# Kernel tuning notes

Hardware: AMD Instinct MI355X
Metric: run time of the kernel (lower is better)

## Reference

```python
import jax, jax.numpy as jnp
import numpy as np

S = 4096          # sequence length (must equal d_model due to the module's v-transpose bug)
D = 4096          # d_model; n_head = heads = 1, bs = 1
SCALE = 64.0      # scale_factor = sqrt(d_model)
W_STD = 0.02      # weight init scale to keep softmax logits sane


def setup_inputs() -> dict:
    k0 = jax.random.key(0)
    ks = jax.random.split(k0, 8)
    return {
        "query": jax.random.normal(ks[0], (1, S, D), jnp.float32),
        "key":   jax.random.normal(ks[1], (1, S, D), jnp.float32),
        "value": jax.random.normal(ks[2], (1, S, D), jnp.float32),
        "Wq": jax.random.normal(ks[3], (D, D), jnp.float32) * W_STD,
        "bq": jnp.zeros((D,), jnp.float32),
        "Wk": jax.random.normal(ks[4], (D, D), jnp.float32) * W_STD,
        "bk": jnp.zeros((D,), jnp.float32),
        "Wv": jax.random.normal(ks[5], (D, D), jnp.float32) * W_STD,
        "bv": jnp.zeros((D,), jnp.float32),
        "Wo": jax.random.normal(ks[6], (D, D), jnp.float32) * W_STD,
        "bo": jnp.zeros((D,), jnp.float32),
    }


def reference(query, key, value, Wq, bq, Wk, bk, Wv, bv, Wo, bo):
    # Linear projections (torch Linear: x @ W.T + b). n_head = 1, so out dim = D.
    q = query @ Wq.T + bq                       # [1, S, D]
    k = key   @ Wk.T + bk                       # [1, S, D]
    v = value @ Wv.T + bv                       # [1, S, D]
    # k.reshape(bs, heads, -1, d_model).transpose(2, 3) -> [1, 1, D, S]
    k4 = k.reshape(1, 1, S, D).transpose(0, 1, 3, 2)
    # v gets the SAME (buggy) transpose -> [1, 1, D, S]
    v4 = v.reshape(1, 1, S, D).transpose(0, 1, 3, 2)
    # q [1,S,D] broadcasts against k4 [1,1,D,S] -> scores [1,1,S,S]
    scores = jnp.matmul(q[:, None], k4) / SCALE
    attn = jax.nn.softmax(scores, axis=-1)      # [1, 1, S, S]
    # dropout_p = 0 / eval mode -> identity
    ctx = jnp.matmul(attn, v4)                  # [1, 1, S, D] (S == D)
    out = ctx @ Wo.T + bo + value[:, None]      # residual add, broadcast to [1,1,S,D]
    return out.reshape(1, -1, D)                # [1, S, D]
```

## Files before the change

### kernel.cpp

```cpp
#include <hip/hip_runtime.h>


typedef __attribute__((ext_vector_type(4))) float f32x4;
typedef __attribute__((ext_vector_type(8))) short short8;
typedef __attribute__((ext_vector_type(4))) unsigned short us4;

#define DIM 4096
#define NT  64

__device__ __forceinline__ unsigned short f2bf(float f) {
    unsigned int u = __builtin_bit_cast(unsigned int, f);
    u += 0x7fffu + ((u >> 16) & 1u);
    return (unsigned short)(u >> 16);
}

__device__ __forceinline__ void gll16(const void* g, void* l) {
    __builtin_amdgcn_global_load_lds(
        (const __attribute__((address_space(1))) unsigned int*)g,
        (__attribute__((address_space(3))) unsigned int*)l,
        16, 0, 0);
}

__global__ void cast_kernel(const float* __restrict__ in, unsigned short* __restrict__ out) {
    const size_t i = ((size_t)blockIdx.x * 256 + threadIdx.x) * 4;
    float4 x = *(const float4*)(in + i);
    us4 y;
    y.x = f2bf(x.x); y.y = f2bf(x.y); y.z = f2bf(x.z); y.w = f2bf(x.w);
    *(us4*)(out + i) = y;
}

template <int EPI>
__global__ __launch_bounds__(512, 2)
void gemm256(const unsigned short* __restrict__ A, const unsigned short* __restrict__ B,
             void* __restrict__ Cout, const float* __restrict__ bias,
             const float* __restrict__ res) {
    __shared__ alignas(16) char lds[131072];

    const int tid = threadIdx.x;
    const int w = tid >> 6, l = tid & 63;
    const int wr = w >> 2, wc = w & 3;

    const int bid = blockIdx.x;
    const int swz = (bid & 7) * 32 + (bid >> 3);
    const int row0 = (swz >> 4) << 8;
    const int col0 = (swz & 15) << 8;

    const int laneA  = (l & 15) * 64 + (((l >> 4) << 4) ^ ((l & 8) << 2));
    const int sl_row = l >> 2;
    const int sl_col = ((l & 3) << 3) ^ ((l & 32) ? 16 : 0);

    f32x4 acc[8][4];
    const f32x4 zero = {0.f, 0.f, 0.f, 0.f};
#pragma unroll
    for (int m = 0; m < 8; ++m)
#pragma unroll
        for (int n = 0; n < 4; ++n) acc[m][n] = zero;

    char* const ldsp = (char*)lds;

    auto stage = [&](const unsigned short* __restrict__ M, char* ldsMat, int rowbase,
                     int t, int h) {
        {
            const int rg = h * 8 + (w >> 1), cg = w & 1;
            gll16(M + (size_t)(rowbase + rg * 16 + sl_row) * DIM + t * 64 + cg * 32 + sl_col,
                  ldsMat + ((rg * 2 + cg) << 10));
        }
        {
            const int s = 8 + w;
            const int rg = h * 8 + (s >> 1), cg = s & 1;
            gll16(M + (size_t)(rowbase + rg * 16 + sl_row) * DIM + t * 64 + cg * 32 + sl_col,
                  ldsMat + ((rg * 2 + cg) << 10));
        }
    };

    stage(A, ldsp,          row0, 0, 0);
    stage(A, ldsp,          row0, 0, 1);
    stage(B, ldsp + 32768,  col0, 0, 0);
    stage(B, ldsp + 32768,  col0, 0, 1);
    stage(A, ldsp + 65536,  row0, 1, 0);
    asm volatile("s_waitcnt vmcnt(2)\ns_barrier" ::: "memory");

#pragma unroll 1
    for (int t = 0; t < NT; ++t) {
        const char* Ab = ldsp + (t & 1) * 65536;
        const char* Bb = Ab + 32768;
        const int t1 = (t + 1 < NT) ? t + 1 : NT - 1;
        const int t2 = (t + 2 < NT) ? t + 2 : NT - 1;
        char* A1 = ldsp + (t1 & 1) * 65536;
        char* B1 = A1 + 32768;
        char* A2 = ldsp + (t2 & 1) * 65536;

        const int aoff = wr * 16384 + laneA;
        const int boff = wc * 8192 + laneA;

        short8 alo[4][2], ahi[4][2], b0[2][2], b1[2][2];

#pragma unroll
        for (int n2 = 0; n2 < 2; ++n2)
#pragma unroll
            for (int ks = 0; ks < 2; ++ks)
                b0[n2][ks] = *(const short8*)(Bb + boff + ((n2 * 2 + ks) << 10));
#pragma unroll
        for (int m2 = 0; m2 < 4; ++m2)
#pragma unroll
            for (int ks = 0; ks < 2; ++ks)
                alo[m2][ks] = *(const short8*)(Ab + aoff + ((m2 * 2 + ks) << 10));
        stage(A, A1, row0, t1, 1);
        __builtin_amdgcn_s_setprio(1);
#pragma unroll
        for (int m2 = 0; m2 < 4; ++m2)
#pragma unroll
            for (int n2 = 0; n2 < 2; ++n2)
#pragma unroll
                for (int ks = 0; ks < 2; ++ks)
                    acc[m2][n2] = __builtin_amdgcn_mfma_f32_16x16x32_bf16(
                        alo[m2][ks], b0[n2][ks], acc[m2][n2], 0, 0, 0);
        __builtin_amdgcn_s_setprio(0);

#pragma unroll
        for (int n2 = 0; n2 < 2; ++n2)
#pragma unroll
            for (int ks = 0; ks < 2; ++ks)
                b1[n2][ks] = *(const short8*)(Bb + boff + (((2 + n2) * 2 + ks) << 10));
#pragma unroll
        for (int m2 = 0; m2 < 4; ++m2)
#pragma unroll
            for (int ks = 0; ks < 2; ++ks)
                ahi[m2][ks] = *(const short8*)(Ab + aoff + (((4 + m2) * 2 + ks) << 10));
        stage(B, B1, col0, t1, 0);
        __builtin_amdgcn_s_setprio(1);
#pragma unroll
        for (int m2 = 0; m2 < 4; ++m2)
#pragma unroll
            for (int n2 = 0; n2 < 2; ++n2)
#pragma unroll
                for (int ks = 0; ks < 2; ++ks)
                    acc[m2][2 + n2] = __builtin_amdgcn_mfma_f32_16x16x32_bf16(
                        alo[m2][ks], b1[n2][ks], acc[m2][2 + n2], 0, 0, 0);
        __builtin_amdgcn_s_setprio(0);

        asm volatile("s_barrier" ::: "memory");

        stage(B, B1, col0, t1, 1);
        __builtin_amdgcn_s_setprio(1);
#pragma unroll
        for (int m2 = 0; m2 < 4; ++m2)
#pragma unroll
            for (int n2 = 0; n2 < 2; ++n2)
#pragma unroll
                for (int ks = 0; ks < 2; ++ks)
                    acc[4 + m2][2 + n2] = __builtin_amdgcn_mfma_f32_16x16x32_bf16(
                        ahi[m2][ks], b1[n2][ks], acc[4 + m2][2 + n2], 0, 0, 0);
        __builtin_amdgcn_s_setprio(0);

        stage(A, A2, row0, t2, 0);
        __builtin_amdgcn_s_setprio(1);
#pragma unroll
        for (int m2 = 0; m2 < 4; ++m2)
#pragma unroll
            for (int n2 = 0; n2 < 2; ++n2)
#pragma unroll
                for (int ks = 0; ks < 2; ++ks)
                    acc[4 + m2][n2] = __builtin_amdgcn_mfma_f32_16x16x32_bf16(
                        ahi[m2][ks], b0[n2][ks], acc[4 + m2][n2], 0, 0, 0);
        __builtin_amdgcn_s_setprio(0);
        asm volatile("s_waitcnt vmcnt(2)\ns_barrier" ::: "memory");
    }
    asm volatile("s_waitcnt vmcnt(0)" ::: "memory");

#pragma unroll
    for (int mf = 0; mf < 8; ++mf) {
        const int grow0 = row0 + wr * 128 + mf * 16 + ((l >> 4) << 2);
#pragma unroll
        for (int nf = 0; nf < 4; ++nf) {
            const int gcol = col0 + wc * 64 + nf * 16 + (l & 15);
            float bias_v = 0.f;
            if constexpr (EPI != 1) {
                if (bias) bias_v = bias[gcol];
            }
#pragma unroll
            for (int r = 0; r < 4; ++r) {
                const size_t idx = (size_t)(grow0 + r) * DIM + gcol;
                const float x = acc[mf][nf][r] + bias_v;
                if constexpr (EPI == 0) {
                    ((unsigned short*)Cout)[idx] = f2bf(x);
                } else if constexpr (EPI == 1) {
                    ((float*)Cout)[idx] = x * 0.015625f;
                } else {
                    ((float*)Cout)[idx] = x + res[idx];
                }
            }
        }
    }
}

__global__ __launch_bounds__(256)
void softmax_kernel(const float* __restrict__ S, unsigned short* __restrict__ P) {
    const int row = blockIdx.x;
    const int t = threadIdx.x;
    const float* src = S + (size_t)row * DIM;

    float v[16];
#pragma unroll
    for (int i = 0; i < 16; ++i) v[i] = src[t + (i << 8)];

    float m = v[0];
#pragma unroll
    for (int i = 1; i < 16; ++i) m = fmaxf(m, v[i]);
#pragma unroll
    for (int off = 32; off > 0; off >>= 1) m = fmaxf(m, __shfl_xor(m, off));

    __shared__ float redm[4], reds[4];
    if ((t & 63) == 0) redm[t >> 6] = m;
    __syncthreads();
    m = fmaxf(fmaxf(redm[0], redm[1]), fmaxf(redm[2], redm[3]));

    float s = 0.f;
#pragma unroll
    for (int i = 0; i < 16; ++i) {
        v[i] = expf(v[i] - m);
        s += v[i];
    }
#pragma unroll
    for (int off = 32; off > 0; off >>= 1) s += __shfl_xor(s, off);
    if ((t & 63) == 0) reds[t >> 6] = s;
    __syncthreads();
    s = (reds[0] + reds[1]) + (reds[2] + reds[3]);

    const float inv = 1.0f / s;
    unsigned short* dst = P + (size_t)row * DIM;
#pragma unroll
    for (int i = 0; i < 16; ++i) dst[t + (i << 8)] = f2bf(v[i] * inv);
}

extern "C" void kernel_launch(void* const* d_in, const int* in_sizes, int n_in,
                              void* d_out, int out_size, void* d_ws, size_t ws_size,
                              hipStream_t stream) {
    const float* query = (const float*)d_in[0];
    const float* key   = (const float*)d_in[1];
    const float* value = (const float*)d_in[2];
    const float* Wq    = (const float*)d_in[3];
    const float* bq    = (const float*)d_in[4];
    const float* Wk    = (const float*)d_in[5];
    const float* bk    = (const float*)d_in[6];
    const float* Wv    = (const float*)d_in[7];
    const float* bv    = (const float*)d_in[8];
    const float* Wo    = (const float*)d_in[9];
    const float* bo    = (const float*)d_in[10];

    const size_t SZ = (size_t)DIM * DIM;
    unsigned short* qb   = (unsigned short*)d_ws;
    unsigned short* kb   = qb + SZ;
    unsigned short* vb   = kb + SZ;
    unsigned short* xb   = vb + SZ;
    unsigned short* wb   = xb + SZ;
    unsigned short* Pb   = wb + SZ;
    unsigned short* ctxb = Pb + SZ;
    float* scores = (float*)(ctxb + SZ);

    const dim3 cg(16384), cb(256);
    const dim3 gg(256), gb(512);

    cast_kernel<<<cg, cb, 0, stream>>>(query, xb);
    cast_kernel<<<cg, cb, 0, stream>>>(Wq, wb);
    gemm256<0><<<gg, gb, 0, stream>>>(xb, wb, qb, bq, nullptr);
    cast_kernel<<<cg, cb, 0, stream>>>(key, xb);
    cast_kernel<<<cg, cb, 0, stream>>>(Wk, wb);
    gemm256<0><<<gg, gb, 0, stream>>>(xb, wb, kb, bk, nullptr);
    cast_kernel<<<cg, cb, 0, stream>>>(value, xb);
    cast_kernel<<<cg, cb, 0, stream>>>(Wv, wb);
    gemm256<0><<<gg, gb, 0, stream>>>(xb, wb, vb, bv, nullptr);
    gemm256<1><<<gg, gb, 0, stream>>>(qb, kb, scores, nullptr, nullptr);
    softmax_kernel<<<4096, 256, 0, stream>>>(scores, Pb);
    gemm256<0><<<gg, gb, 0, stream>>>(Pb, vb, ctxb, nullptr, nullptr);
    cast_kernel<<<cg, cb, 0, stream>>>(Wo, wb);
    gemm256<2><<<gg, gb, 0, stream>>>(ctxb, wb, d_out, bo, value);
}
```

Baseline: 796.1 us.

## Switch GEMM to 32x32x16 bf16 MFMA with matching LDS layout

Replaces the 16x16x32 MFMA tiling with 32x32x16 bf16 MFMA instructions, so each wave holds 4x2 f32x16 accumulators instead of 8x4 f32x4. The global-to-LDS staging layout, the swizzled LDS read offsets and the epilogue row/column mapping are all rewritten to match the 32x32 operand format. The larger MFMA shape is meant to cut the instruction count and the LDS read traffic per FLOP. It also changes the bank-conflict behaviour and register usage.

```diff
diff --git a/kernel.cpp b/kernel.cpp
--- a/kernel.cpp
+++ b/kernel.cpp
@@ -1,7 +1,7 @@
 #include <hip/hip_runtime.h>
 
 
-typedef __attribute__((ext_vector_type(4))) float f32x4;
+typedef __attribute__((ext_vector_type(16))) float f32x16;
 typedef __attribute__((ext_vector_type(8))) short short8;
 typedef __attribute__((ext_vector_type(4))) unsigned short us4;
 
@@ -45,31 +45,30 @@
     const int row0 = (swz >> 4) << 8;
     const int col0 = (swz & 15) << 8;
 
-    const int laneA  = (l & 15) * 64 + (((l >> 4) << 4) ^ ((l & 8) << 2));
-    const int sl_row = l >> 2;
-    const int sl_col = ((l & 3) << 3) ^ ((l & 32) ? 16 : 0);
-
-    f32x4 acc[8][4];
-    const f32x4 zero = {0.f, 0.f, 0.f, 0.f};
-#pragma unroll
-    for (int m = 0; m < 8; ++m)
-#pragma unroll
-        for (int n = 0; n < 4; ++n) acc[m][n] = zero;
+    const int laneR = (l & 31) * 32 + (((l >> 5) ^ (l & 1)) << 4);
+    const int sg_row = l >> 1;
+    const int sg_k   = ((l & 1) ^ ((l >> 1) & 1)) << 3;
+
+    f32x16 acc[4][2];
+#pragma unroll
+    for (int m = 0; m < 4; ++m)
+#pragma unroll
+        for (int n = 0; n < 2; ++n)
+#pragma unroll
+            for (int r = 0; r < 16; ++r) acc[m][n][r] = 0.f;
 
     char* const ldsp = (char*)lds;
 
     auto stage = [&](const unsigned short* __restrict__ M, char* ldsMat, int rowbase,
                      int t, int h) {
-        {
-            const int rg = h * 8 + (w >> 1), cg = w & 1;
-            gll16(M + (size_t)(rowbase + rg * 16 + sl_row) * DIM + t * 64 + cg * 32 + sl_col,
-                  ldsMat + ((rg * 2 + cg) << 10));
-        }
-        {
-            const int s = 8 + w;
-            const int rg = h * 8 + (s >> 1), cg = s & 1;
-            gll16(M + (size_t)(rowbase + rg * 16 + sl_row) * DIM + t * 64 + cg * 32 + sl_col,
-                  ldsMat + ((rg * 2 + cg) << 10));
+        const int R = h * 4 + (w & 3);
+        const int grow = rowbase + R * 32 + sg_row;
+        const int Kg0 = (w >> 2) * 2;
+#pragma unroll
+        for (int j = 0; j < 2; ++j) {
+            const int Kg = Kg0 + j;
+            gll16(M + (size_t)grow * DIM + t * 64 + Kg * 16 + sg_k,
+                  ldsMat + ((R * 4 + Kg) << 10));
         }
     };
 
@@ -90,53 +89,45 @@
         char* B1 = A1 + 32768;
         char* A2 = ldsp + (t2 & 1) * 65536;
 
-        const int aoff = wr * 16384 + laneA;
-        const int boff = wc * 8192 + laneA;
-
-        short8 alo[4][2], ahi[4][2], b0[2][2], b1[2][2];
-
-#pragma unroll
-        for (int n2 = 0; n2 < 2; ++n2)
-#pragma unroll
-            for (int ks = 0; ks < 2; ++ks)
-                b0[n2][ks] = *(const short8*)(Bb + boff + ((n2 * 2 + ks) << 10));
-#pragma unroll
-        for (int m2 = 0; m2 < 4; ++m2)
-#pragma unroll
-            for (int ks = 0; ks < 2; ++ks)
-                alo[m2][ks] = *(const short8*)(Ab + aoff + ((m2 * 2 + ks) << 10));
+        const int aoff = wr * 16384 + laneR;
+        const int boff = wc * 8192 + laneR;
+
+        short8 alo[2][4], ahi[2][4], b0[4], b1[4];
+
+#pragma unroll
+        for (int ks = 0; ks < 4; ++ks)
+            b0[ks] = *(const short8*)(Bb + boff + (ks << 10));
+#pragma unroll
+        for (int mf = 0; mf < 2; ++mf)
+#pragma unroll
+            for (int ks = 0; ks < 4; ++ks)
+                alo[mf][ks] = *(const short8*)(Ab + aoff + (mf << 12) + (ks << 10));
         stage(A, A1, row0, t1, 1);
         __builtin_amdgcn_s_setprio(1);
 #pragma unroll
-        for (int m2 = 0; m2 < 4; ++m2)
-#pragma unroll
-            for (int n2 = 0; n2 < 2; ++n2)
-#pragma unroll
-                for (int ks = 0; ks < 2; ++ks)
-                    acc[m2][n2] = __builtin_amdgcn_mfma_f32_16x16x32_bf16(
-                        alo[m2][ks], b0[n2][ks], acc[m2][n2], 0, 0, 0);
-        __builtin_amdgcn_s_setprio(0);
-
-#pragma unroll
-        for (int n2 = 0; n2 < 2; ++n2)
-#pragma unroll
-            for (int ks = 0; ks < 2; ++ks)
-                b1[n2][ks] = *(const short8*)(Bb + boff + (((2 + n2) * 2 + ks) << 10));
-#pragma unroll
-        for (int m2 = 0; m2 < 4; ++m2)
-#pragma unroll
-            for (int ks = 0; ks < 2; ++ks)
-                ahi[m2][ks] = *(const short8*)(Ab + aoff + (((4 + m2) * 2 + ks) << 10));
+        for (int mf = 0; mf < 2; ++mf)
+#pragma unroll
+            for (int ks = 0; ks < 4; ++ks)
+                acc[mf][0] = __builtin_amdgcn_mfma_f32_32x32x16_bf16(
+                    alo[mf][ks], b0[ks], acc[mf][0], 0, 0, 0);
+        __builtin_amdgcn_s_setprio(0);
+
+#pragma unroll
+        for (int ks = 0; ks < 4; ++ks)
+            b1[ks] = *(const short8*)(Bb + boff + 4096 + (ks << 10));
+#pragma unroll
+        for (int mf = 0; mf < 2; ++mf)
+#pragma unroll
+            for (int ks = 0; ks < 4; ++ks)
+                ahi[mf][ks] = *(const short8*)(Ab + aoff + ((2 + mf) << 12) + (ks << 10));
         stage(B, B1, col0, t1, 0);
         __builtin_amdgcn_s_setprio(1);
 #pragma unroll
-        for (int m2 = 0; m2 < 4; ++m2)
-#pragma unroll
-            for (int n2 = 0; n2 < 2; ++n2)
-#pragma unroll
-                for (int ks = 0; ks < 2; ++ks)
-                    acc[m2][2 + n2] = __builtin_amdgcn_mfma_f32_16x16x32_bf16(
-                        alo[m2][ks], b1[n2][ks], acc[m2][2 + n2], 0, 0, 0);
+        for (int mf = 0; mf < 2; ++mf)
+#pragma unroll
+            for (int ks = 0; ks < 4; ++ks)
+                acc[mf][1] = __builtin_amdgcn_mfma_f32_32x32x16_bf16(
+                    alo[mf][ks], b1[ks], acc[mf][1], 0, 0, 0);
         __builtin_amdgcn_s_setprio(0);
 
         asm volatile("s_barrier" ::: "memory");
@@ -144,44 +135,41 @@
         stage(B, B1, col0, t1, 1);
         __builtin_amdgcn_s_setprio(1);
 #pragma unroll
-        for (int m2 = 0; m2 < 4; ++m2)
-#pragma unroll
-            for (int n2 = 0; n2 < 2; ++n2)
-#pragma unroll
-                for (int ks = 0; ks < 2; ++ks)
-                    acc[4 + m2][2 + n2] = __builtin_amdgcn_mfma_f32_16x16x32_bf16(
-                        ahi[m2][ks], b1[n2][ks], acc[4 + m2][2 + n2], 0, 0, 0);
+        for (int mf = 0; mf < 2; ++mf)
+#pragma unroll
+            for (int ks = 0; ks < 4; ++ks)
+                acc[2 + mf][1] = __builtin_amdgcn_mfma_f32_32x32x16_bf16(
+                    ahi[mf][ks], b1[ks], acc[2 + mf][1], 0, 0, 0);
         __builtin_amdgcn_s_setprio(0);
 
         stage(A, A2, row0, t2, 0);
         __builtin_amdgcn_s_setprio(1);
 #pragma unroll
-        for (int m2 = 0; m2 < 4; ++m2)
-#pragma unroll
-            for (int n2 = 0; n2 < 2; ++n2)
-#pragma unroll
-                for (int ks = 0; ks < 2; ++ks)
-                    acc[4 + m2][n2] = __builtin_amdgcn_mfma_f32_16x16x32_bf16(
-                        ahi[m2][ks], b0[n2][ks], acc[4 + m2][n2], 0, 0, 0);
+        for (int mf = 0; mf < 2; ++mf)
+#pragma unroll
+            for (int ks = 0; ks < 4; ++ks)
+                acc[2 + mf][0] = __builtin_amdgcn_mfma_f32_32x32x16_bf16(
+                    ahi[mf][ks], b0[ks], acc[2 + mf][0], 0, 0, 0);
         __builtin_amdgcn_s_setprio(0);
         asm volatile("s_waitcnt vmcnt(2)\ns_barrier" ::: "memory");
     }
     asm volatile("s_waitcnt vmcnt(0)" ::: "memory");
 
 #pragma unroll
-    for (int mf = 0; mf < 8; ++mf) {
-        const int grow0 = row0 + wr * 128 + mf * 16 + ((l >> 4) << 2);
-#pragma unroll
-        for (int nf = 0; nf < 4; ++nf) {
-            const int gcol = col0 + wc * 64 + nf * 16 + (l & 15);
+    for (int mf = 0; mf < 4; ++mf) {
+        const int grow_b = row0 + wr * 128 + mf * 32 + ((l >> 5) << 2);
+#pragma unroll
+        for (int nf = 0; nf < 2; ++nf) {
+            const int gcol = col0 + wc * 64 + nf * 32 + (l & 31);
             float bias_v = 0.f;
             if constexpr (EPI != 1) {
                 if (bias) bias_v = bias[gcol];
             }
 #pragma unroll
-            for (int r = 0; r < 4; ++r) {
-                const size_t idx = (size_t)(grow0 + r) * DIM + gcol;
-                const float x = acc[mf][nf][r] + bias_v;
+            for (int rg = 0; rg < 16; ++rg) {
+                const int grow = grow_b + (rg & 3) + ((rg >> 2) << 3);
+                const size_t idx = (size_t)grow * DIM + gcol;
+                const float x = acc[mf][nf][rg] + bias_v;
                 if constexpr (EPI == 0) {
                     ((unsigned short*)Cout)[idx] = f2bf(x);
                 } else if constexpr (EPI == 1) {
```

Result: slower. 913.4 us (+14.7%).

## Restructure GEMM main loop to prefetch next tile fragments and double-buffer B registers

Applied to the files above, without the earlier changes.

Reorganizes the bf16 MFMA GEMM main loop into a two-iteration unrolled body. The prologue stages two full K-tiles, and each step loads the next tile's alo/b0 fragments into registers before the final MFMA group. Global-to-LDS staging now targets tile t+2 in the just-consumed buffer, with adjusted waitcnt and barrier placement. The goal is to hide LDS read latency and cut barrier stalls, at the cost of more live registers (an extra b0 set) and a more delicate synchronisation scheme.

```diff
diff --git a/kernel.cpp b/kernel.cpp
--- a/kernel.cpp
+++ b/kernel.cpp
@@ -57,6 +57,13 @@
         for (int n = 0; n < 4; ++n) acc[m][n] = zero;
 
     char* const ldsp = (char*)lds;
+    char* const A0 = ldsp;
+    char* const B0 = ldsp + 32768;
+    char* const A1 = ldsp + 65536;
+    char* const B1 = ldsp + 98304;
+
+    const int aoff = wr * 16384 + laneA;
+    const int boff = wc * 8192 + laneA;
 
     auto stage = [&](const unsigned short* __restrict__ M, char* ldsMat, int rowbase,
                      int t, int h) {
@@ -73,39 +80,38 @@
         }
     };
 
-    stage(A, ldsp,          row0, 0, 0);
-    stage(A, ldsp,          row0, 0, 1);
-    stage(B, ldsp + 32768,  col0, 0, 0);
-    stage(B, ldsp + 32768,  col0, 0, 1);
-    stage(A, ldsp + 65536,  row0, 1, 0);
-    asm volatile("s_waitcnt vmcnt(2)\ns_barrier" ::: "memory");
-
-#pragma unroll 1
-    for (int t = 0; t < NT; ++t) {
-        const char* Ab = ldsp + (t & 1) * 65536;
-        const char* Bb = Ab + 32768;
-        const int t1 = (t + 1 < NT) ? t + 1 : NT - 1;
+    short8 alo[4][2], ahi[4][2], b1[2][2], b0A[2][2], b0B[2][2];
+
+    stage(A, A0, row0, 0, 0); stage(A, A0, row0, 0, 1);
+    stage(B, B0, col0, 0, 0); stage(B, B0, col0, 0, 1);
+    stage(A, A1, row0, 1, 0); stage(A, A1, row0, 1, 1);
+    stage(B, B1, col0, 1, 0); stage(B, B1, col0, 1, 1);
+    asm volatile("s_waitcnt vmcnt(8)\ns_barrier" ::: "memory");
+#pragma unroll
+    for (int m2 = 0; m2 < 4; ++m2)
+#pragma unroll
+        for (int ks = 0; ks < 2; ++ks)
+            alo[m2][ks] = *(const short8*)(A0 + aoff + ((m2 * 2 + ks) << 10));
+#pragma unroll
+    for (int n2 = 0; n2 < 2; ++n2)
+#pragma unroll
+        for (int ks = 0; ks < 2; ++ks)
+            b0A[n2][ks] = *(const short8*)(B0 + boff + ((n2 * 2 + ks) << 10));
+
+    auto body = [&](int t, char* Abuf, char* Bbuf, const char* An, const char* Bn,
+                    short8 (&b0c)[2][2], short8 (&b0n)[2][2]) {
         const int t2 = (t + 2 < NT) ? t + 2 : NT - 1;
-        char* A1 = ldsp + (t1 & 1) * 65536;
-        char* B1 = A1 + 32768;
-        char* A2 = ldsp + (t2 & 1) * 65536;
-
-        const int aoff = wr * 16384 + laneA;
-        const int boff = wc * 8192 + laneA;
-
-        short8 alo[4][2], ahi[4][2], b0[2][2], b1[2][2];
 
 #pragma unroll
         for (int n2 = 0; n2 < 2; ++n2)
 #pragma unroll
             for (int ks = 0; ks < 2; ++ks)
-                b0[n2][ks] = *(const short8*)(Bb + boff + ((n2 * 2 + ks) << 10));
-#pragma unroll
-        for (int m2 = 0; m2 < 4; ++m2)
-#pragma unroll
-            for (int ks = 0; ks < 2; ++ks)
-                alo[m2][ks] = *(const short8*)(Ab + aoff + ((m2 * 2 + ks) << 10));
-        stage(A, A1, row0, t1, 1);
+                b1[n2][ks] = *(const short8*)(Bbuf + boff + (((2 + n2) * 2 + ks) << 10));
+#pragma unroll
+        for (int m2 = 0; m2 < 4; ++m2)
+#pragma unroll
+            for (int ks = 0; ks < 2; ++ks)
+                ahi[m2][ks] = *(const short8*)(Abuf + aoff + (((4 + m2) * 2 + ks) << 10));
         __builtin_amdgcn_s_setprio(1);
 #pragma unroll
         for (int m2 = 0; m2 < 4; ++m2)
@@ -114,20 +120,12 @@
 #pragma unroll
                 for (int ks = 0; ks < 2; ++ks)
                     acc[m2][n2] = __builtin_amdgcn_mfma_f32_16x16x32_bf16(
-                        alo[m2][ks], b0[n2][ks], acc[m2][n2], 0, 0, 0);
-        __builtin_amdgcn_s_setprio(0);
-
-#pragma unroll
-        for (int n2 = 0; n2 < 2; ++n2)
-#pragma unroll
-            for (int ks = 0; ks < 2; ++ks)
-                b1[n2][ks] = *(const short8*)(Bb + boff + (((2 + n2) * 2 + ks) << 10));
-#pragma unroll
-        for (int m2 = 0; m2 < 4; ++m2)
-#pragma unroll
-            for (int ks = 0; ks < 2; ++ks)
-                ahi[m2][ks] = *(const short8*)(Ab + aoff + (((4 + m2) * 2 + ks) << 10));
-        stage(B, B1, col0, t1, 0);
+                        alo[m2][ks], b0c[n2][ks], acc[m2][n2], 0, 0, 0);
+        __builtin_amdgcn_s_setprio(0);
+        asm volatile("s_barrier" ::: "memory");
+
+        stage(A, Abuf, row0, t2, 0);
+        stage(A, Abuf, row0, t2, 1);
         __builtin_amdgcn_s_setprio(1);
 #pragma unroll
         for (int m2 = 0; m2 < 4; ++m2)
@@ -139,9 +137,7 @@
                         alo[m2][ks], b1[n2][ks], acc[m2][2 + n2], 0, 0, 0);
         __builtin_amdgcn_s_setprio(0);
 
-        asm volatile("s_barrier" ::: "memory");
-
-        stage(B, B1, col0, t1, 1);
+        stage(B, Bbuf, col0, t2, 0);
         __builtin_amdgcn_s_setprio(1);
 #pragma unroll
         for (int m2 = 0; m2 < 4; ++m2)
@@ -152,8 +148,19 @@
                     acc[4 + m2][2 + n2] = __builtin_amdgcn_mfma_f32_16x16x32_bf16(
                         ahi[m2][ks], b1[n2][ks], acc[4 + m2][2 + n2], 0, 0, 0);
         __builtin_amdgcn_s_setprio(0);
-
-        stage(A, A2, row0, t2, 0);
+        asm volatile("s_waitcnt vmcnt(6)\ns_barrier" ::: "memory");
+
+#pragma unroll
+        for (int m2 = 0; m2 < 4; ++m2)
+#pragma unroll
+            for (int ks = 0; ks < 2; ++ks)
+                alo[m2][ks] = *(const short8*)(An + aoff + ((m2 * 2 + ks) << 10));
+#pragma unroll
+        for (int n2 = 0; n2 < 2; ++n2)
+#pragma unroll
+            for (int ks = 0; ks < 2; ++ks)
+                b0n[n2][ks] = *(const short8*)(Bn + boff + ((n2 * 2 + ks) << 10));
+        stage(B, Bbuf, col0, t2, 1);
         __builtin_amdgcn_s_setprio(1);
 #pragma unroll
         for (int m2 = 0; m2 < 4; ++m2)
@@ -162,9 +169,15 @@
 #pragma unroll
                 for (int ks = 0; ks < 2; ++ks)
                     acc[4 + m2][n2] = __builtin_amdgcn_mfma_f32_16x16x32_bf16(
-                        ahi[m2][ks], b0[n2][ks], acc[4 + m2][n2], 0, 0, 0);
-        __builtin_amdgcn_s_setprio(0);
-        asm volatile("s_waitcnt vmcnt(2)\ns_barrier" ::: "memory");
+                        ahi[m2][ks], b0c[n2][ks], acc[4 + m2][n2], 0, 0, 0);
+        __builtin_amdgcn_s_setprio(0);
+    };
+
+#pragma unroll 1
+    for (int tt = 0; tt < NT / 2; ++tt) {
+        const int t = 2 * tt;
+        body(t,     A0, B0, A1, B1, b0A, b0B);
+        body(t + 1, A1, B1, A0, B0, b0B, b0A);
     }
     asm volatile("s_waitcnt vmcnt(0)" ::: "memory");
 
```

Result: no change. 806.5 us (+1.3%).
